# Performance work log

Hardware: AMD Instinct MI355X
Metric: run time of the kernel (lower is better)

Reference implementation:

```python
import jax, jax.numpy as jnp
import numpy as np

N = 10000        # num_nodes
F_IN = 256       # dataset_num_features
H = 128          # hidden_channels
C_OUT = 40       # dataset_num_classes
L = 3            # num_layers
HEADS = 8
DH = H // HEADS  # per-head dim
E = 160000       # num edges (before self loops)
SCALE = 1.0 / float(np.sqrt(DH))


def setup_inputs() -> dict:
    key = jax.random.key(0)
    ks = jax.random.split(key, 8)
    s = lambda k, *sh: (jax.random.normal(k, sh, dtype=jnp.float32) * 0.05)
    return dict(
        edge_index=jax.random.randint(ks[0], (2, E), 0, N, dtype=jnp.int32),
        x_param=s(ks[1], N, F_IN),
        lin1_w=s(ks[2], F_IN, H),
        lin1_b=jnp.zeros((H,), jnp.float32),
        wq=s(ks[3], L, H, H),
        wk=s(ks[4], L, H, H),
        wv=s(ks[5], L, H, H),
        bq=jnp.zeros((L, H), jnp.float32),
        bk=jnp.zeros((L, H), jnp.float32),
        bv=jnp.zeros((L, H), jnp.float32),
        lin2_w=s(ks[6], H, C_OUT),
        lin2_b=jnp.zeros((C_OUT,), jnp.float32),
    )


def _gcn_norm(edge_index):
    # PyG gcn_norm: add self loops (weight 1), symmetric D^-1/2 A D^-1/2
    loops = jnp.arange(N, dtype=edge_index.dtype)
    row = jnp.concatenate([edge_index[0], loops])  # source j
    col = jnp.concatenate([edge_index[1], loops])  # target i
    deg = jax.ops.segment_sum(jnp.ones(row.shape, jnp.float32), col, num_segments=N)
    dis = jnp.where(deg > 0, jax.lax.rsqrt(jnp.maximum(deg, 1e-12)), 0.0)
    return row, col, dis[row] * dis[col]


def _restricted_softmax(score):
    # softmax with an implicit extra logit at `margin=0`
    m = jnp.maximum(jnp.max(score, axis=-1, keepdims=True), 0.0)
    e = jnp.exp(score - m)
    return e / (jnp.sum(e, axis=-1, keepdims=True) + jnp.exp(-m))


def _forward(edge_index, x_param, lin1_w, lin1_b, wq, wk, wv, bq, bk, bv, lin2_w, lin2_b):
    row, col, norm = _gcn_norm(edge_index)
    # dropouts are eval-mode no-ops
    x = jax.nn.relu(x_param @ lin1_w + lin1_b)  # [N, H]
    x_all = x[:, None, :]                       # [N, 1, H]
    for l in range(L):
        t = x_all.shape[1]
        # project per-node first (linear commutes with per-edge gather)
        q = (x_all[:, -1] @ wq[l] + bq[l]).reshape(N, HEADS, DH)      # query from latest state
        k = (x_all @ wk[l] + bk[l]).reshape(N, t, HEADS, DH)          # keys over full history
        v = (x_all @ wv[l] + bv[l]).reshape(N, t, HEADS, DH)
        qe = q[col]   # [Etot, heads, dh]   (x_i)
        ke = k[row]   # [Etot, t, heads, dh] (x_j)
        ve = v[row]
        score = jnp.einsum('ehd,ethd->eht', qe, ke) * SCALE
        attn = _restricted_softmax(score)        # attention-dropout is a no-op in eval
        msg = jnp.einsum('eht,ethd->ehd', attn, ve).reshape(-1, H) * norm[:, None]
        out = jax.ops.segment_sum(msg, col, num_segments=N)  # aggr='add'
        x = jax.nn.relu(out)
        x_all = jnp.concatenate([x_all, x[:, None, :]], axis=1)
    logits = x_all[:, -1] @ lin2_w + lin2_b
    return jax.nn.log_softmax(logits, axis=1)


def reference(edge_index, x_param, lin1_w, lin1_b, wq, wk, wv, bq, bk, bv, lin2_w, lin2_b):
    return _forward(edge_index, x_param, lin1_w, lin1_b, wq, wk, wv, bq, bk, bv, lin2_w, lin2_b)
```

## Files before the change

kernel.cpp:

```cpp
#include <hip/hip_runtime.h>
#include <math.h>

#define N_NODES 10000
#define F_IN_D  256
#define H_DIM   128
#define C_OUTD  40
#define NHEADS  8
#define NEDGES  160000
#define ETOT    (NEDGES + N_NODES)
#define SCALE_F 0.25f
#define TILES_N 157
#define KVSZ    ((size_t)N_NODES * 3 * 256)

typedef __attribute__((ext_vector_type(8))) short bf16x8;
typedef __attribute__((ext_vector_type(4))) float f32x4;
typedef __attribute__((ext_vector_type(2))) float f32x2;

__device__ __forceinline__ unsigned short f2bf(float f) {
    unsigned int u = __float_as_uint(f);
    unsigned int r = (u + 0x7FFFu + ((u >> 16) & 1u)) >> 16;
    return (unsigned short)r;
}
__device__ __forceinline__ float bf2f(unsigned short h) {
    return __uint_as_float(((unsigned int)h) << 16);
}
__device__ __forceinline__ unsigned char f2fp8(float v) {
    int pk = __builtin_amdgcn_cvt_pk_fp8_f32(v, v, 0, false);
    return (unsigned char)(pk & 0xff);
}


__global__ void k_prep(const float* __restrict__ w1, const float* __restrict__ wq,
                       const float* __restrict__ wk, const float* __restrict__ wv,
                       const float* __restrict__ w2, const int* __restrict__ col,
                       unsigned short* __restrict__ W1T, unsigned short* __restrict__ WTq,
                       unsigned short* __restrict__ WTk, unsigned short* __restrict__ WTv,
                       unsigned short* __restrict__ W2T, int* __restrict__ degi) {
    int b = blockIdx.x;
    if (b < 728) {
        int e = b * 256 + threadIdx.x;
        if (e < 32768) {
            int n = e >> 8, k = e & 255;
            W1T[e] = f2bf(w1[k * H_DIM + n]);
        } else if (e < 180224) {
            int e2 = e - 32768;
            int mat = e2 >> 14;
            int r   = e2 & 16383;
            int n = r >> 7, k = r & 127;
            int l = mat / 3, ws = mat % 3;
            const float*    src = (ws == 0) ? wq  : (ws == 1) ? wk  : wv;
            unsigned short* dst = (ws == 0) ? WTq : (ws == 1) ? WTk : WTv;
            dst[l * 16384 + n * H_DIM + k] = f2bf(src[l * 16384 + k * H_DIM + n]);
        } else if (e < 186368) {
            int e3 = e - 180224;
            int c = e3 >> 7, k = e3 & 127;
            W2T[c * H_DIM + k] = (c < C_OUTD) ? f2bf(w2[k * C_OUTD + c]) : 0;
        }
    } else {
        int e = (b - 728) * 256 + threadIdx.x;
        if (e < NEDGES) atomicAdd(&degi[col[e]], 1);
    }
}


__device__ __forceinline__ void lin1_block(int bid, const float* __restrict__ X,
                                           const unsigned short* __restrict__ W1T,
                                           const float* __restrict__ b1,
                                           unsigned short* __restrict__ X0, int nct) {
    int tid = threadIdx.x;
    int wid = tid >> 6, lane = tid & 63;
    int m = lane & 15, quad = lane >> 4;
    int rowA = bid * 64 + wid * 16 + m;
    int rowc = rowA < N_NODES ? rowA : N_NODES - 1;
    bf16x8 af[8];
    const float* ap = X + (size_t)rowc * F_IN_D + quad * 8;
    #pragma unroll
    for (int s = 0; s < 8; ++s) {
        float4 lo = *(const float4*)(ap + s * 32);
        float4 hi = *(const float4*)(ap + s * 32 + 4);
        union { unsigned short u[8]; bf16x8 v; } pk;
        pk.u[0] = f2bf(lo.x); pk.u[1] = f2bf(lo.y);
        pk.u[2] = f2bf(lo.z); pk.u[3] = f2bf(lo.w);
        pk.u[4] = f2bf(hi.x); pk.u[5] = f2bf(hi.y);
        pk.u[6] = f2bf(hi.z); pk.u[7] = f2bf(hi.w);
        af[s] = pk.v;
    }
    int row0 = bid * 64 + wid * 16 + quad * 4;
    for (int ct = 0; ct < nct; ++ct) {
        int col = ct * 16 + m;
        const unsigned short* bp = W1T + (size_t)col * F_IN_D + quad * 8;
        f32x4 acc = {0.f, 0.f, 0.f, 0.f};
        #pragma unroll
        for (int s = 0; s < 8; ++s) {
            bf16x8 bfr = __builtin_bit_cast(bf16x8, *(const uint4*)(bp + s * 32));
            acc = __builtin_amdgcn_mfma_f32_16x16x32_bf16(af[s], bfr, acc, 0, 0, 0);
        }
        float bb = b1[col];
        #pragma unroll
        for (int rg = 0; rg < 4; ++rg) {
            int r = row0 + rg;
            if (r < N_NODES)
                X0[(size_t)r * H_DIM + col] = f2bf(fmaxf(acc[rg] + bb, 0.f));
        }
    }
}

__device__ __forceinline__ void qkv_block(int mi, int rt,
                                          const unsigned short* __restrict__ XHb,
                                          const unsigned short* __restrict__ WTq_l,
                                          const unsigned short* __restrict__ WTk_l,
                                          const unsigned short* __restrict__ WTv_l,
                                          const float* __restrict__ bq_l,
                                          const float* __restrict__ bk_l,
                                          const float* __restrict__ bv_l,
                                          unsigned short* __restrict__ Qb,
                                          unsigned char* __restrict__ KVb,
                                          int hasQ, int qslice, int nK, int sbase, int nct) {
    int tid = threadIdx.x;
    int wid = tid >> 6, lane = tid & 63;
    int m = lane & 15, quad = lane >> 4;
    const unsigned short* WT; const float* bias; int slice, mode;
    if (hasQ && mi == 0) { WT = WTq_l; bias = bq_l; slice = qslice; mode = 0; }
    else {
        int j = mi - hasQ;
        if (j < nK) { WT = WTk_l; bias = bk_l; slice = sbase + j;      mode = 1; }
        else        { WT = WTv_l; bias = bv_l; slice = sbase + j - nK; mode = 2; }
    }
    const unsigned short* A = XHb + (size_t)slice * N_NODES * H_DIM;
    int rowA = rt * 64 + wid * 16 + m;
    bf16x8 af[4];
    const unsigned short* ap = A + (size_t)rowA * H_DIM + quad * 8;
    #pragma unroll
    for (int s = 0; s < 4; ++s)
        af[s] = __builtin_bit_cast(bf16x8, *(const uint4*)(ap + s * 32));
    int row0 = rt * 64 + wid * 16 + quad * 4;
    int vofs = (mode == 2) ? 8 : 0;
    for (int cp = 0; cp < nct; ++cp) {
        int colA = cp * 32 + m;
        int colB = colA + 16;
        const unsigned short* bpA = WT + (size_t)colA * H_DIM + quad * 8;
        const unsigned short* bpB = WT + (size_t)colB * H_DIM + quad * 8;
        bf16x8 bA[4], bB[4];
        #pragma unroll
        for (int s = 0; s < 4; ++s) {
            bA[s] = __builtin_bit_cast(bf16x8, *(const uint4*)(bpA + s * 32));
            bB[s] = __builtin_bit_cast(bf16x8, *(const uint4*)(bpB + s * 32));
        }
        f32x4 accA = {0.f, 0.f, 0.f, 0.f};
        f32x4 accB = {0.f, 0.f, 0.f, 0.f};
        #pragma unroll
        for (int s = 0; s < 4; ++s) {
            accA = __builtin_amdgcn_mfma_f32_16x16x32_bf16(af[s], bA[s], accA, 0, 0, 0);
            accB = __builtin_amdgcn_mfma_f32_16x16x32_bf16(af[s], bB[s], accB, 0, 0, 0);
        }
        float bbA = bias[colA], bbB = bias[colB];
        #pragma unroll
        for (int rg = 0; rg < 4; ++rg) {
            int r = row0 + rg;
            if (r < N_NODES) {
                float vA = accA[rg] + bbA;
                float vB = accB[rg] + bbB;
                if (mode == 0) {
                    Qb[(size_t)r * H_DIM + colA] = f2bf(vA);
                    Qb[(size_t)r * H_DIM + colB] = f2bf(vB);
                } else {
                    size_t nb = ((size_t)r * 3 + slice) * 256;
                    KVb[nb + (colA >> 3) * 16 + (colA & 7) + vofs] = f2fp8(vA);
                    KVb[nb + (colB >> 3) * 16 + (colB & 7) + vofs] = f2fp8(vB);
                }
            }
        }
    }
}


template <int T>
__device__ __forceinline__ void kv_load(const uint4* __restrict__ KV, int r, int ci,
                                        uint4 (&kv)[T]) {
    const uint4* p = KV + (size_t)r * 48 + ci;
    #pragma unroll
    for (int s = 0; s < T; ++s) kv[s] = p[s * 16];
}

template <int T>
__device__ __forceinline__ void edge_accum(const uint4 (&kv)[T], const float (&q)[8],
                                           float nrm, float (&a)[8]) {
    float sc[T];
    #pragma unroll
    for (int s = 0; s < T; ++s) {
        f32x2 k0 = __builtin_amdgcn_cvt_pk_f32_fp8(kv[s].x, false);
        f32x2 k1 = __builtin_amdgcn_cvt_pk_f32_fp8(kv[s].x, true);
        f32x2 k2 = __builtin_amdgcn_cvt_pk_f32_fp8(kv[s].y, false);
        f32x2 k3 = __builtin_amdgcn_cvt_pk_f32_fp8(kv[s].y, true);
        float p = q[0] * k0[0] + q[1] * k0[1] + q[2] * k1[0] + q[3] * k1[1]
                + q[4] * k2[0] + q[5] * k2[1] + q[6] * k3[0] + q[7] * k3[1];
        p += __shfl_xor(p, 1, 2);
        sc[s] = p;
    }
    float m = 0.f;
    #pragma unroll
    for (int s = 0; s < T; ++s) m = fmaxf(m, sc[s]);
    float den = __expf(-m);
    float mv[8];
    #pragma unroll
    for (int i = 0; i < 8; ++i) mv[i] = 0.f;
    #pragma unroll
    for (int s = 0; s < T; ++s) {
        float w = __expf(sc[s] - m);
        den += w;
        f32x2 v0 = __builtin_amdgcn_cvt_pk_f32_fp8(kv[s].z, false);
        f32x2 v1 = __builtin_amdgcn_cvt_pk_f32_fp8(kv[s].z, true);
        f32x2 v2 = __builtin_amdgcn_cvt_pk_f32_fp8(kv[s].w, false);
        f32x2 v3 = __builtin_amdgcn_cvt_pk_f32_fp8(kv[s].w, true);
        mv[0] += w * v0[0]; mv[1] += w * v0[1];
        mv[2] += w * v1[0]; mv[3] += w * v1[1];
        mv[4] += w * v2[0]; mv[5] += w * v2[1];
        mv[6] += w * v3[0]; mv[7] += w * v3[1];
    }
    float ws = __fdividef(nrm, den);
    #pragma unroll
    for (int i = 0; i < 8; ++i) a[i] += ws * mv[i];
}

template <int T>
__device__ __forceinline__ void attn_block(int bid, const unsigned short* __restrict__ Q,
                                           const uint4* __restrict__ KV,
                                           const int* __restrict__ csr_row,
                                           const float* __restrict__ csr_norm,
                                           const int* __restrict__ offsets,
                                           const int* __restrict__ degi,
                                           unsigned int* __restrict__ Xout) {
    int tid = threadIdx.x;
    int wid = tid >> 6, lane = tid & 63;
    int quarter = lane >> 4, ci = lane & 15;
    int n = bid * 4 + wid;
    float q[8];
    {
        uint4 qp = *(const uint4*)&Q[(size_t)n * H_DIM + ci * 8];
        q[0] = __uint_as_float(qp.x << 16) * SCALE_F;
        q[1] = __uint_as_float(qp.x & 0xffff0000u) * SCALE_F;
        q[2] = __uint_as_float(qp.y << 16) * SCALE_F;
        q[3] = __uint_as_float(qp.y & 0xffff0000u) * SCALE_F;
        q[4] = __uint_as_float(qp.z << 16) * SCALE_F;
        q[5] = __uint_as_float(qp.z & 0xffff0000u) * SCALE_F;
        q[6] = __uint_as_float(qp.w << 16) * SCALE_F;
        q[7] = __uint_as_float(qp.w & 0xffff0000u) * SCALE_F;
    }
    int start = offsets[n];
    int cnt   = degi[n];
    int nq = (cnt + 3) >> 2;
    float a[8];
    #pragma unroll
    for (int i = 0; i < 8; ++i) a[i] = 0.f;

    auto rowload = [&](int j, int& r, float& nrm) {
        int j4 = j * 4 + quarter;
        int valid = j4 < cnt;
        int idx = start + (valid ? j4 : 0);
        r = csr_row[idx];
        nrm = valid ? csr_norm[idx] : 0.f;
    };

    int r0; float nCUR; rowload(0, r0, nCUR);
    int rN; float nN;   rowload(1, rN, nN);
    uint4 kvA[T], kvB[T];
    kv_load<T>(KV, r0, ci, kvA);

    int j = 0;
    for (;;) {
        {
            int r2; float n2; rowload(j + 2, r2, n2);
            kv_load<T>(KV, rN, ci, kvB);
            edge_accum<T>(kvA, q, nCUR, a);
            nCUR = nN; rN = r2; nN = n2;
        }
        if (++j >= nq) break;
        {
            int r2; float n2; rowload(j + 2, r2, n2);
            kv_load<T>(KV, rN, ci, kvA);
            edge_accum<T>(kvB, q, nCUR, a);
            nCUR = nN; rN = r2; nN = n2;
        }
        if (++j >= nq) break;
    }

    #pragma unroll
    for (int i = 0; i < 8; ++i) {
        a[i] += __shfl_xor(a[i], 16, 64);
        a[i] += __shfl_xor(a[i], 32, 64);
    }
    if (quarter == 0) {
        uint4 o;
        o.x = ((unsigned int)f2bf(fmaxf(a[1], 0.f)) << 16) | (unsigned int)f2bf(fmaxf(a[0], 0.f));
        o.y = ((unsigned int)f2bf(fmaxf(a[3], 0.f)) << 16) | (unsigned int)f2bf(fmaxf(a[2], 0.f));
        o.z = ((unsigned int)f2bf(fmaxf(a[5], 0.f)) << 16) | (unsigned int)f2bf(fmaxf(a[4], 0.f));
        o.w = ((unsigned int)f2bf(fmaxf(a[7], 0.f)) << 16) | (unsigned int)f2bf(fmaxf(a[6], 0.f));
        *(uint4*)&Xout[(size_t)n * 64 + ci * 4] = o;
    }
}


__global__ __launch_bounds__(256) void k_scan_lin1(int* __restrict__ degi,
                                                   int* __restrict__ offsets,
                                                   const float* __restrict__ X,
                                                   const unsigned short* __restrict__ W1T,
                                                   const float* __restrict__ b1,
                                                   unsigned short* __restrict__ X0, int nct) {
    if (blockIdx.x == 0) {
        __shared__ int part[256];
        int tid = threadIdx.x;
        int s = 0;
        if (tid < 250) {
            const int4* d4 = (const int4*)degi;
            for (int i = 0; i < 10; ++i) {
                int4 v = d4[tid * 10 + i];
                s += v.x + v.y + v.z + v.w + 4;
            }
        }
        part[tid] = s;
        __syncthreads();
        for (int off = 1; off < 256; off <<= 1) {
            int v = 0;
            if (tid >= off) v = part[tid - off];
            __syncthreads();
            part[tid] += v;
            __syncthreads();
        }
        if (tid < 250) {
            int base = part[tid] - s;
            int beg = tid * 40;
            for (int i = 0; i < 40; ++i) {
                int d = degi[beg + i] + 1;
                offsets[beg + i] = base;
                degi[beg + i]    = d;
                base += d;
            }
        }
        return;
    }
    lin1_block(blockIdx.x - 1, X, W1T, b1, X0, nct);
}

__global__ __launch_bounds__(256) void k_scatter_qkv0(const int* __restrict__ row,
                                                      const int* __restrict__ col,
                                                      const int* __restrict__ degi,
                                                      const int* __restrict__ offsets,
                                                      int* __restrict__ cursor,
                                                      int* __restrict__ csr_row,
                                                      float* __restrict__ csr_norm,
                                                      const unsigned short* __restrict__ XHb,
                                                      const unsigned short* __restrict__ WTq,
                                                      const unsigned short* __restrict__ WTk,
                                                      const unsigned short* __restrict__ WTv,
                                                      const float* __restrict__ bq,
                                                      const float* __restrict__ bk,
                                                      const float* __restrict__ bv,
                                                      unsigned short* __restrict__ Qb,
                                                      unsigned char* __restrict__ KVb,
                                                      int nct) {
    if (blockIdx.x < 665) {
        int e = blockIdx.x * 256 + threadIdx.x;
        if (e >= ETOT) return;
        int r, c;
        if (e < NEDGES) { r = row[e]; c = col[e]; }
        else            { r = c = e - NEDGES; }
        int slot = offsets[c] + atomicAdd(&cursor[c], 1);
        float dr = rsqrtf((float)degi[r]);
        float dc = rsqrtf((float)degi[c]);
        csr_row[slot]  = r;
        csr_norm[slot] = dr * dc;
        return;
    }
    int b = blockIdx.x - 665;
    qkv_block(b / TILES_N, b % TILES_N, XHb, WTq, WTk, WTv, bq, bk, bv,
              Qb, KVb, 1, 0, 1, 0, nct);
}

template <int T>
__global__ __launch_bounds__(256) void k_attn_qkvold(const unsigned short* __restrict__ Q,
                                                     const uint4* __restrict__ KV,
                                                     const int* __restrict__ csr_row,
                                                     const float* __restrict__ csr_norm,
                                                     const int* __restrict__ offsets,
                                                     const int* __restrict__ degi,
                                                     unsigned int* __restrict__ Xout,
                                                     const unsigned short* __restrict__ XHb,
                                                     const unsigned short* __restrict__ WTk_l,
                                                     const unsigned short* __restrict__ WTv_l,
                                                     const float* __restrict__ bk_l,
                                                     const float* __restrict__ bv_l,
                                                     unsigned char* __restrict__ KVnext,
                                                     int nK, int nct) {
    if (blockIdx.x < 2500) {
        attn_block<T>(blockIdx.x, Q, KV, csr_row, csr_norm, offsets, degi, Xout);
        return;
    }
    int b = blockIdx.x - 2500;
    qkv_block(b / TILES_N, b % TILES_N, XHb, nullptr, WTk_l, WTv_l,
              nullptr, bk_l, bv_l, nullptr, KVnext, 0, 0, nK, 0, nct);
}

__global__ __launch_bounds__(256) void k_qkv(const unsigned short* __restrict__ XHb,
                                             const unsigned short* __restrict__ WTq_l,
                                             const unsigned short* __restrict__ WTk_l,
                                             const unsigned short* __restrict__ WTv_l,
                                             const float* __restrict__ bq_l,
                                             const float* __restrict__ bk_l,
                                             const float* __restrict__ bv_l,
                                             unsigned short* __restrict__ Qb,
                                             unsigned char* __restrict__ KVb,
                                             int qslice, int nct) {
    qkv_block(blockIdx.x / TILES_N, blockIdx.x % TILES_N, XHb, WTq_l, WTk_l, WTv_l,
              bq_l, bk_l, bv_l, Qb, KVb, 1, qslice, 1, qslice, nct);
}

template <int T>
__global__ __launch_bounds__(256) void k_attn_agg(const unsigned short* __restrict__ Q,
                                                  const uint4* __restrict__ KV,
                                                  const int* __restrict__ csr_row,
                                                  const float* __restrict__ csr_norm,
                                                  const int* __restrict__ offsets,
                                                  const int* __restrict__ degi,
                                                  unsigned int* __restrict__ Xout) {
    attn_block<T>(blockIdx.x, Q, KV, csr_row, csr_norm, offsets, degi, Xout);
}


__global__ __launch_bounds__(256) void k_lin2_mfma(const unsigned short* __restrict__ X,
                                                   const unsigned short* __restrict__ W2T,
                                                   const float* __restrict__ b2,
                                                   float* __restrict__ out) {
    int tid = threadIdx.x;
    int wid = tid >> 6, lane = tid & 63;
    int m = lane & 15, quad = lane >> 4;
    int rowA = blockIdx.x * 64 + wid * 16 + m;
    bf16x8 af[4];
    const unsigned short* ap = X + (size_t)rowA * H_DIM + quad * 8;
    #pragma unroll
    for (int s = 0; s < 4; ++s)
        af[s] = __builtin_bit_cast(bf16x8, *(const uint4*)(ap + s * 32));

    f32x4 acc0 = {0.f, 0.f, 0.f, 0.f};
    f32x4 acc1 = {0.f, 0.f, 0.f, 0.f};
    f32x4 acc2 = {0.f, 0.f, 0.f, 0.f};
    const unsigned short* bp0 = W2T + (size_t)(m)      * H_DIM + quad * 8;
    const unsigned short* bp1 = W2T + (size_t)(16 + m) * H_DIM + quad * 8;
    const unsigned short* bp2 = W2T + (size_t)(32 + m) * H_DIM + quad * 8;
    #pragma unroll
    for (int s = 0; s < 4; ++s) {
        bf16x8 b0 = __builtin_bit_cast(bf16x8, *(const uint4*)(bp0 + s * 32));
        acc0 = __builtin_amdgcn_mfma_f32_16x16x32_bf16(af[s], b0, acc0, 0, 0, 0);
        bf16x8 b1 = __builtin_bit_cast(bf16x8, *(const uint4*)(bp1 + s * 32));
        acc1 = __builtin_amdgcn_mfma_f32_16x16x32_bf16(af[s], b1, acc1, 0, 0, 0);
        bf16x8 b2f = __builtin_bit_cast(bf16x8, *(const uint4*)(bp2 + s * 32));
        acc2 = __builtin_amdgcn_mfma_f32_16x16x32_bf16(af[s], b2f, acc2, 0, 0, 0);
    }

    float bb0 = b2[m], bb1 = b2[16 + m];
    float bb2 = (m < 8) ? b2[32 + m] : 0.f;
    int row0 = blockIdx.x * 64 + wid * 16 + quad * 4;
    #pragma unroll
    for (int rg = 0; rg < 4; ++rg) {
        int r = row0 + rg;
        float v0 = acc0[rg] + bb0;
        float v1 = acc1[rg] + bb1;
        float v2 = (m < 8) ? (acc2[rg] + bb2) : -INFINITY;
        float mx = fmaxf(fmaxf(v0, v1), v2);
        #pragma unroll
        for (int o = 8; o > 0; o >>= 1) mx = fmaxf(mx, __shfl_xor(mx, o, 16));
        float sm = __expf(v0 - mx) + __expf(v1 - mx) + ((m < 8) ? __expf(v2 - mx) : 0.f);
        #pragma unroll
        for (int o = 8; o > 0; o >>= 1) sm += __shfl_xor(sm, o, 16);
        float lse = mx + __logf(sm);
        if (r < N_NODES) {
            out[(size_t)r * C_OUTD + m]      = v0 - lse;
            out[(size_t)r * C_OUTD + 16 + m] = v1 - lse;
            if (m < 8) out[(size_t)r * C_OUTD + 32 + m] = v2 - lse;
        }
    }
}


extern "C" void kernel_launch(void* const* d_in, const int* in_sizes, int n_in,
                              void* d_out, int out_size, void* d_ws, size_t ws_size,
                              hipStream_t stream) {
    const int*   ei      = (const int*)d_in[0];
    const int*   row     = ei;
    const int*   col     = ei + NEDGES;
    const float* x_param = (const float*)d_in[1];
    const float* lin1_w  = (const float*)d_in[2];
    const float* lin1_b  = (const float*)d_in[3];
    const float* wq      = (const float*)d_in[4];
    const float* wk      = (const float*)d_in[5];
    const float* wv      = (const float*)d_in[6];
    const float* bq      = (const float*)d_in[7];
    const float* bk      = (const float*)d_in[8];
    const float* bv      = (const float*)d_in[9];
    const float* lin2_w  = (const float*)d_in[10];
    const float* lin2_b  = (const float*)d_in[11];
    float*       out     = (float*)d_out;

    char* wbase = (char*)d_ws;
    size_t off = 0;
    auto alloc = [&](size_t bytes) -> void* {
        off = (off + 255) & ~(size_t)255;
        void* p = wbase + off;
        off += bytes;
        return p;
    };
    int*            degi     = (int*)           alloc((size_t)N_NODES * 4);
    int*            cursor   = (int*)           alloc((size_t)N_NODES * 4);
    int*            offsets  = (int*)           alloc((size_t)N_NODES * 4);
    int*            csr_row  = (int*)           alloc((size_t)ETOT * 4);
    float*          csr_norm = (float*)         alloc((size_t)ETOT * 4);
    unsigned short* W1T      = (unsigned short*)alloc((size_t)H_DIM * F_IN_D * 2);
    unsigned short* WTq      = (unsigned short*)alloc((size_t)3 * H_DIM * H_DIM * 2);
    unsigned short* WTk      = (unsigned short*)alloc((size_t)3 * H_DIM * H_DIM * 2);
    unsigned short* WTv      = (unsigned short*)alloc((size_t)3 * H_DIM * H_DIM * 2);
    unsigned short* W2T      = (unsigned short*)alloc((size_t)48 * H_DIM * 2);
    unsigned short* XHb      = (unsigned short*)alloc((size_t)4 * N_NODES * H_DIM * 2);
    unsigned short* Qb       = (unsigned short*)alloc((size_t)N_NODES * H_DIM * 2);
    unsigned char*  KVb      = (unsigned char*) alloc(2 * KVSZ);

    hipMemsetAsync(degi, 0,
                   (size_t)((char*)(cursor + N_NODES) - (char*)degi), stream);
    k_prep<<<1353, 256, 0, stream>>>(lin1_w, wq, wk, wv, lin2_w, col,
                                     W1T, WTq, WTk, WTv, W2T, degi);

    k_scan_lin1<<<158, 256, 0, stream>>>(degi, offsets, x_param, W1T, lin1_b, XHb, 8);

    k_scatter_qkv0<<<665 + 3 * TILES_N, 256, 0, stream>>>(
        row, col, degi, offsets, cursor, csr_row, csr_norm,
        XHb, WTq, WTk, WTv, bq, bk, bv, Qb, KVb, 4);

    unsigned int* X1 = (unsigned int*)(XHb + (size_t)1 * N_NODES * H_DIM);
    unsigned int* X2 = (unsigned int*)(XHb + (size_t)2 * N_NODES * H_DIM);
    unsigned int* X3 = (unsigned int*)(XHb + (size_t)3 * N_NODES * H_DIM);

    k_attn_qkvold<1><<<2500 + 2 * TILES_N, 256, 0, stream>>>(
        Qb, (const uint4*)KVb, csr_row, csr_norm, offsets, degi, X1,
        XHb, WTk + 16384, WTv + 16384, bk + H_DIM, bv + H_DIM,
        KVb + KVSZ, 1, 4);

    k_qkv<<<3 * TILES_N, 256, 0, stream>>>(
        XHb, WTq + 16384, WTk + 16384, WTv + 16384,
        bq + H_DIM, bk + H_DIM, bv + H_DIM, Qb, KVb + KVSZ, 1, 4);

    k_attn_qkvold<2><<<2500 + 4 * TILES_N, 256, 0, stream>>>(
        Qb, (const uint4*)(KVb + KVSZ), csr_row, csr_norm, offsets, degi, X2,
        XHb, WTk + 2 * 16384, WTv + 2 * 16384, bk + 2 * H_DIM, bv + 2 * H_DIM,
        KVb, 2, 4);

    k_qkv<<<3 * TILES_N, 256, 0, stream>>>(
        XHb, WTq + 2 * 16384, WTk + 2 * 16384, WTv + 2 * 16384,
        bq + 2 * H_DIM, bk + 2 * H_DIM, bv + 2 * H_DIM, Qb, KVb, 2, 4);

    k_attn_agg<3><<<2500, 256, 0, stream>>>(Qb, (const uint4*)KVb, csr_row,
                                            csr_norm, offsets, degi, X3);

    k_lin2_mfma<<<TILES_N, 256, 0, stream>>>(XHb + (size_t)3 * N_NODES * H_DIM,
                                             W2T, lin2_b, out);
}
```

Baseline: 236.5 us.

## Remap attention lanes to full heads over 8 edges and pack CSR entries

Each lane in the attention kernel now owns a whole 16-dim head (8 lanes per node head set) and a wave processes 8 edges at a time instead of 4. This removes the per-score cross-lane shuffle, and each lane issues two 16-byte loads per history slot. The restricted softmax drops the running-max subtraction and computes exp(score) directly with an implicit 1 in the denominator. This saves a pass but can overflow if scores become large. The query scale factor is folded into the Q projection epilogue, and CSR row indices and norms are packed into one int2 array so each edge needs a single load.

Result: slower. 243.4 us (+2.9%).

```diff
diff --git a/kernel.cpp b/kernel.cpp
--- a/kernel.cpp
+++ b/kernel.cpp
@@ -20,9 +20,6 @@
     unsigned int u = __float_as_uint(f);
     unsigned int r = (u + 0x7FFFu + ((u >> 16) & 1u)) >> 16;
     return (unsigned short)r;
-}
-__device__ __forceinline__ float bf2f(unsigned short h) {
-    return __uint_as_float(((unsigned int)h) << 16);
 }
 __device__ __forceinline__ unsigned char f2fp8(float v) {
     int pk = __builtin_amdgcn_cvt_pk_fp8_f32(v, v, 0, false);
@@ -161,8 +158,8 @@
                 float vA = accA[rg] + bbA;
                 float vB = accB[rg] + bbB;
                 if (mode == 0) {
-                    Qb[(size_t)r * H_DIM + colA] = f2bf(vA);
-                    Qb[(size_t)r * H_DIM + colB] = f2bf(vB);
+                    Qb[(size_t)r * H_DIM + colA] = f2bf(vA * SCALE_F);
+                    Qb[(size_t)r * H_DIM + colB] = f2bf(vB * SCALE_F);
                 } else {
                     size_t nb = ((size_t)r * 3 + slice) * 256;
                     KVb[nb + (colA >> 3) * 16 + (colA & 7) + vofs] = f2fp8(vA);
@@ -175,127 +172,142 @@
 
 
 template <int T>
-__device__ __forceinline__ void kv_load(const uint4* __restrict__ KV, int r, int ci,
-                                        uint4 (&kv)[T]) {
-    const uint4* p = KV + (size_t)r * 48 + ci;
-    #pragma unroll
-    for (int s = 0; s < T; ++s) kv[s] = p[s * 16];
+__device__ __forceinline__ void kv_load8(const uint4* __restrict__ KV, int r, int hd,
+                                         uint4 (&kv)[2 * T]) {
+    const uint4* p = KV + (size_t)r * 48 + 2 * hd;
+    #pragma unroll
+    for (int s = 0; s < T; ++s) {
+        kv[2 * s]     = p[s * 16];
+        kv[2 * s + 1] = p[s * 16 + 1];
+    }
 }
 
 template <int T>
-__device__ __forceinline__ void edge_accum(const uint4 (&kv)[T], const float (&q)[8],
-                                           float nrm, float (&a)[8]) {
-    float sc[T];
+__device__ __forceinline__ void edge_accum8(const uint4 (&kv)[2 * T], const float (&q)[16],
+                                            float nrm, float (&a)[16]) {
+    float den = 1.f;
+    float mv[16];
+    #pragma unroll
+    for (int i = 0; i < 16; ++i) mv[i] = 0.f;
     #pragma unroll
     for (int s = 0; s < T; ++s) {
-        f32x2 k0 = __builtin_amdgcn_cvt_pk_f32_fp8(kv[s].x, false);
-        f32x2 k1 = __builtin_amdgcn_cvt_pk_f32_fp8(kv[s].x, true);
-        f32x2 k2 = __builtin_amdgcn_cvt_pk_f32_fp8(kv[s].y, false);
-        f32x2 k3 = __builtin_amdgcn_cvt_pk_f32_fp8(kv[s].y, true);
-        float p = q[0] * k0[0] + q[1] * k0[1] + q[2] * k1[0] + q[3] * k1[1]
-                + q[4] * k2[0] + q[5] * k2[1] + q[6] * k3[0] + q[7] * k3[1];
-        p += __shfl_xor(p, 1, 2);
-        sc[s] = p;
-    }
-    float m = 0.f;
-    #pragma unroll
-    for (int s = 0; s < T; ++s) m = fmaxf(m, sc[s]);
-    float den = __expf(-m);
-    float mv[8];
-    #pragma unroll
-    for (int i = 0; i < 8; ++i) mv[i] = 0.f;
-    #pragma unroll
-    for (int s = 0; s < T; ++s) {
-        float w = __expf(sc[s] - m);
+        uint4 g0 = kv[2 * s], g1 = kv[2 * s + 1];
+        f32x2 k0 = __builtin_amdgcn_cvt_pk_f32_fp8(g0.x, false);
+        f32x2 k1 = __builtin_amdgcn_cvt_pk_f32_fp8(g0.x, true);
+        f32x2 k2 = __builtin_amdgcn_cvt_pk_f32_fp8(g0.y, false);
+        f32x2 k3 = __builtin_amdgcn_cvt_pk_f32_fp8(g0.y, true);
+        f32x2 k4 = __builtin_amdgcn_cvt_pk_f32_fp8(g1.x, false);
+        f32x2 k5 = __builtin_amdgcn_cvt_pk_f32_fp8(g1.x, true);
+        f32x2 k6 = __builtin_amdgcn_cvt_pk_f32_fp8(g1.y, false);
+        f32x2 k7 = __builtin_amdgcn_cvt_pk_f32_fp8(g1.y, true);
+        float p = q[0]  * k0[0] + q[1]  * k0[1] + q[2]  * k1[0] + q[3]  * k1[1]
+                + q[4]  * k2[0] + q[5]  * k2[1] + q[6]  * k3[0] + q[7]  * k3[1]
+                + q[8]  * k4[0] + q[9]  * k4[1] + q[10] * k5[0] + q[11] * k5[1]
+                + q[12] * k6[0] + q[13] * k6[1] + q[14] * k7[0] + q[15] * k7[1];
+        float w = __expf(p);
         den += w;
-        f32x2 v0 = __builtin_amdgcn_cvt_pk_f32_fp8(kv[s].z, false);
-        f32x2 v1 = __builtin_amdgcn_cvt_pk_f32_fp8(kv[s].z, true);
-        f32x2 v2 = __builtin_amdgcn_cvt_pk_f32_fp8(kv[s].w, false);
-        f32x2 v3 = __builtin_amdgcn_cvt_pk_f32_fp8(kv[s].w, true);
-        mv[0] += w * v0[0]; mv[1] += w * v0[1];
-        mv[2] += w * v1[0]; mv[3] += w * v1[1];
-        mv[4] += w * v2[0]; mv[5] += w * v2[1];
-        mv[6] += w * v3[0]; mv[7] += w * v3[1];
+        f32x2 v0 = __builtin_amdgcn_cvt_pk_f32_fp8(g0.z, false);
+        f32x2 v1 = __builtin_amdgcn_cvt_pk_f32_fp8(g0.z, true);
+        f32x2 v2 = __builtin_amdgcn_cvt_pk_f32_fp8(g0.w, false);
+        f32x2 v3 = __builtin_amdgcn_cvt_pk_f32_fp8(g0.w, true);
+        f32x2 v4 = __builtin_amdgcn_cvt_pk_f32_fp8(g1.z, false);
+        f32x2 v5 = __builtin_amdgcn_cvt_pk_f32_fp8(g1.z, true);
+        f32x2 v6 = __builtin_amdgcn_cvt_pk_f32_fp8(g1.w, false);
+        f32x2 v7 = __builtin_amdgcn_cvt_pk_f32_fp8(g1.w, true);
+        mv[0]  += w * v0[0]; mv[1]  += w * v0[1];
+        mv[2]  += w * v1[0]; mv[3]  += w * v1[1];
+        mv[4]  += w * v2[0]; mv[5]  += w * v2[1];
+        mv[6]  += w * v3[0]; mv[7]  += w * v3[1];
+        mv[8]  += w * v4[0]; mv[9]  += w * v4[1];
+        mv[10] += w * v5[0]; mv[11] += w * v5[1];
+        mv[12] += w * v6[0]; mv[13] += w * v6[1];
+        mv[14] += w * v7[0]; mv[15] += w * v7[1];
     }
     float ws = __fdividef(nrm, den);
     #pragma unroll
-    for (int i = 0; i < 8; ++i) a[i] += ws * mv[i];
+    for (int i = 0; i < 16; ++i) a[i] += ws * mv[i];
 }
 
 template <int T>
 __device__ __forceinline__ void attn_block(int bid, const unsigned short* __restrict__ Q,
                                            const uint4* __restrict__ KV,
-                                           const int* __restrict__ csr_row,
-                                           const float* __restrict__ csr_norm,
+                                           const int2* __restrict__ csr,
                                            const int* __restrict__ offsets,
                                            const int* __restrict__ degi,
                                            unsigned int* __restrict__ Xout) {
     int tid = threadIdx.x;
     int wid = tid >> 6, lane = tid & 63;
-    int quarter = lane >> 4, ci = lane & 15;
+    int oct = lane >> 3, hd = lane & 7;
     int n = bid * 4 + wid;
-    float q[8];
+    float q[16];
     {
-        uint4 qp = *(const uint4*)&Q[(size_t)n * H_DIM + ci * 8];
-        q[0] = __uint_as_float(qp.x << 16) * SCALE_F;
-        q[1] = __uint_as_float(qp.x & 0xffff0000u) * SCALE_F;
-        q[2] = __uint_as_float(qp.y << 16) * SCALE_F;
-        q[3] = __uint_as_float(qp.y & 0xffff0000u) * SCALE_F;
-        q[4] = __uint_as_float(qp.z << 16) * SCALE_F;
-        q[5] = __uint_as_float(qp.z & 0xffff0000u) * SCALE_F;
-        q[6] = __uint_as_float(qp.w << 16) * SCALE_F;
-        q[7] = __uint_as_float(qp.w & 0xffff0000u) * SCALE_F;
+        const uint4* qp4 = (const uint4*)&Q[(size_t)n * H_DIM + hd * 16];
+        uint4 qa = qp4[0], qb = qp4[1];
+        q[0]  = __uint_as_float(qa.x << 16); q[1]  = __uint_as_float(qa.x & 0xffff0000u);
+        q[2]  = __uint_as_float(qa.y << 16); q[3]  = __uint_as_float(qa.y & 0xffff0000u);
+        q[4]  = __uint_as_float(qa.z << 16); q[5]  = __uint_as_float(qa.z & 0xffff0000u);
+        q[6]  = __uint_as_float(qa.w << 16); q[7]  = __uint_as_float(qa.w & 0xffff0000u);
+        q[8]  = __uint_as_float(qb.x << 16); q[9]  = __uint_as_float(qb.x & 0xffff0000u);
+        q[10] = __uint_as_float(qb.y << 16); q[11] = __uint_as_float(qb.y & 0xffff0000u);
+        q[12] = __uint_as_float(qb.z << 16); q[13] = __uint_as_float(qb.z & 0xffff0000u);
+        q[14] = __uint_as_float(qb.w << 16); q[15] = __uint_as_float(qb.w & 0xffff0000u);
     }
     int start = offsets[n];
     int cnt   = degi[n];
-    int nq = (cnt + 3) >> 2;
-    float a[8];
-    #pragma unroll
-    for (int i = 0; i < 8; ++i) a[i] = 0.f;
+    int nq = (cnt + 7) >> 3;
+    float a[16];
+    #pragma unroll
+    for (int i = 0; i < 16; ++i) a[i] = 0.f;
 
     auto rowload = [&](int j, int& r, float& nrm) {
-        int j4 = j * 4 + quarter;
-        int valid = j4 < cnt;
-        int idx = start + (valid ? j4 : 0);
-        r = csr_row[idx];
-        nrm = valid ? csr_norm[idx] : 0.f;
+        int j8 = j * 8 + oct;
+        int valid = j8 < cnt;
+        int idx = start + (valid ? j8 : 0);
+        int2 e = csr[idx];
+        r = e.x;
+        nrm = valid ? __int_as_float(e.y) : 0.f;
     };
 
     int r0; float nCUR; rowload(0, r0, nCUR);
     int rN; float nN;   rowload(1, rN, nN);
-    uint4 kvA[T], kvB[T];
-    kv_load<T>(KV, r0, ci, kvA);
+    uint4 kvA[2 * T], kvB[2 * T];
+    kv_load8<T>(KV, r0, hd, kvA);
 
     int j = 0;
     for (;;) {
         {
             int r2; float n2; rowload(j + 2, r2, n2);
-            kv_load<T>(KV, rN, ci, kvB);
-            edge_accum<T>(kvA, q, nCUR, a);
+            kv_load8<T>(KV, rN, hd, kvB);
+            edge_accum8<T>(kvA, q, nCUR, a);
             nCUR = nN; rN = r2; nN = n2;
         }
         if (++j >= nq) break;
         {
             int r2; float n2; rowload(j + 2, r2, n2);
-            kv_load<T>(KV, rN, ci, kvA);
-            edge_accum<T>(kvB, q, nCUR, a);
+            kv_load8<T>(KV, rN, hd, kvA);
+            edge_accum8<T>(kvB, q, nCUR, a);
             nCUR = nN; rN = r2; nN = n2;
         }
         if (++j >= nq) break;
     }
 
     #pragma unroll
-    for (int i = 0; i < 8; ++i) {
+    for (int i = 0; i < 16; ++i) {
+        a[i] += __shfl_xor(a[i], 8, 64);
         a[i] += __shfl_xor(a[i], 16, 64);
         a[i] += __shfl_xor(a[i], 32, 64);
     }
-    if (quarter == 0) {
-        uint4 o;
-        o.x = ((unsigned int)f2bf(fmaxf(a[1], 0.f)) << 16) | (unsigned int)f2bf(fmaxf(a[0], 0.f));
-        o.y = ((unsigned int)f2bf(fmaxf(a[3], 0.f)) << 16) | (unsigned int)f2bf(fmaxf(a[2], 0.f));
-        o.z = ((unsigned int)f2bf(fmaxf(a[5], 0.f)) << 16) | (unsigned int)f2bf(fmaxf(a[4], 0.f));
-        o.w = ((unsigned int)f2bf(fmaxf(a[7], 0.f)) << 16) | (unsigned int)f2bf(fmaxf(a[6], 0.f));
-        *(uint4*)&Xout[(size_t)n * 64 + ci * 4] = o;
+    if (oct == 0) {
+        unsigned int o[8];
+        #pragma unroll
+        for (int i = 0; i < 8; ++i)
+            o[i] = ((unsigned int)f2bf(fmaxf(a[2 * i + 1], 0.f)) << 16)
+                 |  (unsigned int)f2bf(fmaxf(a[2 * i], 0.f));
+        uint4 o0, o1;
+        o0.x = o[0]; o0.y = o[1]; o0.z = o[2]; o0.w = o[3];
+        o1.x = o[4]; o1.y = o[5]; o1.z = o[6]; o1.w = o[7];
+        *(uint4*)&Xout[(size_t)n * 64 + hd * 8]     = o0;
+        *(uint4*)&Xout[(size_t)n * 64 + hd * 8 + 4] = o1;
     }
 }
 
@@ -346,8 +358,7 @@
                                                       const int* __restrict__ degi,
                                                       const int* __restrict__ offsets,
                                                       int* __restrict__ cursor,
-                                                      int* __restrict__ csr_row,
-                                                      float* __restrict__ csr_norm,
+                                                      int2* __restrict__ csr,
                                                       const unsigned short* __restrict__ XHb,
                                                       const unsigned short* __restrict__ WTq,
                                                       const unsigned short* __restrict__ WTk,
@@ -367,8 +378,8 @@
         int slot = offsets[c] + atomicAdd(&cursor[c], 1);
         float dr = rsqrtf((float)degi[r]);
         float dc = rsqrtf((float)degi[c]);
-        csr_row[slot]  = r;
-        csr_norm[slot] = dr * dc;
+        int2 ent; ent.x = r; ent.y = __float_as_int(dr * dc);
+        csr[slot] = ent;
         return;
     }
     int b = blockIdx.x - 665;
@@ -379,8 +390,7 @@
 template <int T>
 __global__ __launch_bounds__(256) void k_attn_qkvold(const unsigned short* __restrict__ Q,
                                                      const uint4* __restrict__ KV,
-                                                     const int* __restrict__ csr_row,
-                                                     const float* __restrict__ csr_norm,
+                                                     const int2* __restrict__ csr,
                                                      const int* __restrict__ offsets,
                                                      const int* __restrict__ degi,
                                                      unsigned int* __restrict__ Xout,
@@ -392,7 +402,7 @@
                                                      unsigned char* __restrict__ KVnext,
                                                      int nK, int nct) {
     if (blockIdx.x < 2500) {
-        attn_block<T>(blockIdx.x, Q, KV, csr_row, csr_norm, offsets, degi, Xout);
+        attn_block<T>(blockIdx.x, Q, KV, csr, offsets, degi, Xout);
         return;
     }
     int b = blockIdx.x - 2500;
@@ -417,12 +427,11 @@
 template <int T>
 __global__ __launch_bounds__(256) void k_attn_agg(const unsigned short* __restrict__ Q,
                                                   const uint4* __restrict__ KV,
-                                                  const int* __restrict__ csr_row,
-                                                  const float* __restrict__ csr_norm,
+                                                  const int2* __restrict__ csr,
                                                   const int* __restrict__ offsets,
                                                   const int* __restrict__ degi,
                                                   unsigned int* __restrict__ Xout) {
-    attn_block<T>(blockIdx.x, Q, KV, csr_row, csr_norm, offsets, degi, Xout);
+    attn_block<T>(blockIdx.x, Q, KV, csr, offsets, degi, Xout);
 }
 
 
@@ -511,8 +520,7 @@
     int*            degi     = (int*)           alloc((size_t)N_NODES * 4);
     int*            cursor   = (int*)           alloc((size_t)N_NODES * 4);
     int*            offsets  = (int*)           alloc((size_t)N_NODES * 4);
-    int*            csr_row  = (int*)           alloc((size_t)ETOT * 4);
-    float*          csr_norm = (float*)         alloc((size_t)ETOT * 4);
+    int2*           csr      = (int2*)          alloc((size_t)ETOT * 8);
     unsigned short* W1T      = (unsigned short*)alloc((size_t)H_DIM * F_IN_D * 2);
     unsigned short* WTq      = (unsigned short*)alloc((size_t)3 * H_DIM * H_DIM * 2);
     unsigned short* WTk      = (unsigned short*)alloc((size_t)3 * H_DIM * H_DIM * 2);
@@ -530,7 +538,7 @@
     k_scan_lin1<<<158, 256, 0, stream>>>(degi, offsets, x_param, W1T, lin1_b, XHb, 8);
 
     k_scatter_qkv0<<<665 + 3 * TILES_N, 256, 0, stream>>>(
-        row, col, degi, offsets, cursor, csr_row, csr_norm,
+        row, col, degi, offsets, cursor, csr,
         XHb, WTq, WTk, WTv, bq, bk, bv, Qb, KVb, 4);
 
     unsigned int* X1 = (unsigned int*)(XHb + (size_t)1 * N_NODES * H_DIM);
@@ -538,7 +546,7 @@
     unsigned int* X3 = (unsigned int*)(XHb + (size_t)3 * N_NODES * H_DIM);
 
     k_attn_qkvold<1><<<2500 + 2 * TILES_N, 256, 0, stream>>>(
-        Qb, (const uint4*)KVb, csr_row, csr_norm, offsets, degi, X1,
+        Qb, (const uint4*)KVb, csr, offsets, degi, X1,
         XHb, WTk + 16384, WTv + 16384, bk + H_DIM, bv + H_DIM,
         KVb + KVSZ, 1, 4);
 
@@ -547,7 +555,7 @@
         bq + H_DIM, bk + H_DIM, bv + H_DIM, Qb, KVb + KVSZ, 1, 4);
 
     k_attn_qkvold<2><<<2500 + 4 * TILES_N, 256, 0, stream>>>(
-        Qb, (const uint4*)(KVb + KVSZ), csr_row, csr_norm, offsets, degi, X2,
+        Qb, (const uint4*)(KVb + KVSZ), csr, offsets, degi, X2,
         XHb, WTk + 2 * 16384, WTv + 2 * 16384, bk + 2 * H_DIM, bv + 2 * H_DIM,
         KVb, 2, 4);
 
@@ -555,8 +563,8 @@
         XHb, WTq + 2 * 16384, WTk + 2 * 16384, WTv + 2 * 16384,
         bq + 2 * H_DIM, bk + 2 * H_DIM, bv + 2 * H_DIM, Qb, KVb, 2, 4);
 
-    k_attn_agg<3><<<2500, 256, 0, stream>>>(Qb, (const uint4*)KVb, csr_row,
-                                            csr_norm, offsets, degi, X3);
+    k_attn_agg<3><<<2500, 256, 0, stream>>>(Qb, (const uint4*)KVb, csr,
+                                            offsets, degi, X3);
 
     k_lin2_mfma<<<TILES_N, 256, 0, stream>>>(XHb + (size_t)3 * N_NODES * H_DIM,
                                              W2T, lin2_b, out);
```
